# Optimization experiments

Measured on AMD Instinct MI355X. Metric: run time of the kernel, lower is better.

## Reference

```python
import jax, jax.numpy as jnp
import numpy as np

N_NODES = 50000


def spmm(rows, cols, vals, dense):
    # out[i,:] = sum_{e: rows[e]==i} vals[e] * dense[cols[e], :]
    gathered = dense[cols] * vals[:, None]  # [E, D]
    return jax.ops.segment_sum(gathered, rows, num_segments=N_NODES)


def setup_inputs() -> dict:
    key = jax.random.key(0)
    k1, k2, k3, k4, k5, k6 = jax.random.split(key, 6)
    N, E, F, H, C = N_NODES, 800000, 512, 256, 64
    node_features = jax.random.normal(k1, (N, F), dtype=jnp.float32)
    adj_rows = jax.random.randint(k2, (E,), 0, N, dtype=jnp.int32)
    adj_cols = jax.random.randint(k3, (E,), 0, N, dtype=jnp.int32)
    adj_vals = jax.random.uniform(k4, (E,), dtype=jnp.float32)
    W1 = jax.random.normal(k5, (F, H), dtype=jnp.float32) * (1.0 / np.sqrt(F))
    b1 = jnp.zeros((H,), dtype=jnp.float32)
    W2 = jax.random.normal(k6, (H, C), dtype=jnp.float32) * (1.0 / np.sqrt(H))
    b2 = jnp.zeros((C,), dtype=jnp.float32)
    return {"node_features": node_features, "adj_rows": adj_rows,
            "adj_cols": adj_cols, "adj_vals": adj_vals,
            "W1": W1, "b1": b1, "W2": W2, "b2": b2}


def reference(node_features, adj_rows, adj_cols, adj_vals, W1, b1, W2, b2):
    # Layer 1: dense projection then sparse aggregation, then ReLU.
    support1 = node_features @ W1 + b1           # [N, H]
    x = jax.nn.relu(spmm(adj_rows, adj_cols, adj_vals, support1))
    # Dropout is identity in eval mode (training=False).
    # Layer 2
    support2 = x @ W2 + b2                       # [N, C]
    x = spmm(adj_rows, adj_cols, adj_vals, support2)
    return jax.nn.log_softmax(x, axis=1)
```

## Files before the change

kernel.cpp:

```cpp
#include <hip/hip_runtime.h>

#define N_NODES 50000
#define N_EDGES 800000
#define F_IN    512
#define H_DIM   256
#define C_DIM   64
#define MPAD    50048

#define NB      196
#define NCHUNK  196
#define CHUNK   4096
#define BCAP    6144

typedef __bf16 bf16;
typedef __bf16 bf16x4 __attribute__((ext_vector_type(4)));
typedef __bf16 bf16x8 __attribute__((ext_vector_type(8)));
typedef float  f32x4  __attribute__((ext_vector_type(4)));
typedef unsigned int u32;
typedef unsigned long long u64;
typedef unsigned char u8;

__device__ __forceinline__ void gl_lds16(const void* g, void* l) {
    __builtin_amdgcn_global_load_lds(
        (const __attribute__((address_space(1))) u32*)g,
        (__attribute__((address_space(3))) u32*)l, 16, 0, 0);
}

__device__ __forceinline__ float unpack_val(u32 pk) {
    return __builtin_bit_cast(float, pk << 16);
}


__global__ __launch_bounds__(1024) void prep_k(const int* __restrict__ rows,
                                               const float* __restrict__ W1,
                                               const float* __restrict__ W2,
                                               u32* __restrict__ G,
                                               bf16* __restrict__ W1t,
                                               bf16* __restrict__ W2t) {
    __shared__ u32 h[16 * NB];
    int bid = blockIdx.x, tid = threadIdx.x;
    if (bid < NCHUNK) {
        int wid = tid >> 6;
        for (int i = tid; i < 16 * NB; i += 1024) h[i] = 0;
        __syncthreads();
        int base = bid * CHUNK;
        int end = base + CHUNK; if (end > N_EDGES) end = N_EDGES;
        for (int e = base + tid; e < end; e += 1024)
            atomicAdd(&h[wid * NB + (rows[e] >> 8)], 1);
        __syncthreads();
        if (tid < NB) {
            u32 s = 0;
#pragma unroll
            for (int w = 0; w < 16; w++) s += h[w * NB + tid];
            G[tid * NCHUNK + bid] = s;
        }
    } else {
        int i = (bid - NCHUNK) * 1024 + tid;
        if (i < F_IN * H_DIM) {
            int k = i >> 8, n = i & 255;
            W1t[n * F_IN + k] = (bf16)W1[i];
        } else {
            int j = i - F_IN * H_DIM;
            if (j < H_DIM * C_DIM) {
                int k = j >> 6, n = j & 63;
                W2t[n * H_DIM + k] = (bf16)W2[j];
            }
        }
    }
}


__global__ __launch_bounds__(512) void sg_k(const int* __restrict__ rows,
                                            const int* __restrict__ cols,
                                            const float* __restrict__ vals,
                                            const u32* __restrict__ G,
                                            u32* __restrict__ epack,
                                            u8* __restrict__ lrow,
                                            const float* __restrict__ A,
                                            const bf16* __restrict__ Bt,
                                            const float* __restrict__ bias,
                                            bf16* __restrict__ C) {
    __shared__ __attribute__((aligned(16))) char smem[49152];
    int bid = blockIdx.x, tid = threadIdx.x;
    int wid = tid >> 6, lane = tid & 63;

    if (bid < NCHUNK) {
        u32* sdat  = (u32*)smem;
        u8*  sbkt  = (u8*)(smem + 16384);
        u8*  srow  = (u8*)(smem + 20480);
        u32* h     = (u32*)(smem + 24576);
        u32* loff  = (u32*)(smem + 32768);
        u32* lcur  = (u32*)(smem + 33792);
        u32* gbase = (u32*)(smem + 34816);
        u32* wt    = (u32*)(smem + 35840);
        int c = bid;
        int base = c * CHUNK;
        int end = base + CHUNK; if (end > N_EDGES) end = N_EDGES;
        int n = end - base;

        for (int i = tid; i < 2048; i += 512) h[i] = 0;

        u32 tot = 0, pre = 0, incl = 0;
        if (tid < 256) {
            if (tid < NB) {
                for (int cc = 0; cc < NCHUNK; cc++) {
                    u32 v = G[tid * NCHUNK + cc];
                    tot += v;
                    if (cc < c) pre += v;
                }
            }
            incl = tot;
#pragma unroll
            for (int off = 1; off < 64; off <<= 1) {
                u32 u = __shfl_up(incl, off, 64);
                if (lane >= off) incl += u;
            }
            if (lane == 63) wt[wid] = incl;
        }
        __syncthreads();
        if (tid < 256) {
            u32 wpre = 0;
#pragma unroll
            for (int w = 0; w < 4; w++)
                if (w < wid) wpre += wt[w];
            if (tid < NB) gbase[tid] = (wpre + incl - tot) + pre;
        }

        u32 pk_r[8], b_r[8], lr_r[8];
#pragma unroll
        for (int j = 0; j < 8; j++) {
            int e = base + tid + j * 512;
            bool ok = e < end;
            int ee = ok ? e : base;
            int r = rows[ee];
            unsigned short vb = __builtin_bit_cast(unsigned short, (bf16)vals[ee]);
            pk_r[j] = ((u32)cols[ee] << 16) | (u32)vb;
            b_r[j] = (u32)(r >> 8);
            lr_r[j] = (u32)(r & 255);
            if (ok) atomicAdd(&h[wid * 256 + b_r[j]], 1);
        }
        __syncthreads();

        u32 t2 = 0, incl2 = 0;
        if (tid < 256) {
#pragma unroll
            for (int w2 = 0; w2 < 8; w2++) t2 += h[w2 * 256 + tid];
            incl2 = t2;
#pragma unroll
            for (int off = 1; off < 64; off <<= 1) {
                u32 u = __shfl_up(incl2, off, 64);
                if (lane >= off) incl2 += u;
            }
            if (lane == 63) wt[wid] = incl2;
        }
        __syncthreads();
        if (tid < 256) {
            u32 wpre2 = 0;
#pragma unroll
            for (int w = 0; w < 4; w++)
                if (w < wid) wpre2 += wt[w];
            u32 excl = wpre2 + incl2 - t2;
            loff[tid] = excl;
            lcur[tid] = excl;
        }
        __syncthreads();

#pragma unroll
        for (int j = 0; j < 8; j++) {
            int e = base + tid + j * 512;
            if (e < end) {
                u32 p = atomicAdd(&lcur[b_r[j]], 1);
                sdat[p] = pk_r[j];
                sbkt[p] = (u8)b_r[j];
                srow[p] = (u8)lr_r[j];
            }
        }
        __syncthreads();

        for (int i = tid; i < n; i += 512) {
            u32 b2 = sbkt[i];
            u32 dst = gbase[b2] + (u32)i - loff[b2];
            epack[dst] = sdat[i];
            lrow[dst] = srow[i];
        }
        return;
    }

    constexpr int BM = 128, BK = 64;
    bf16* As = (bf16*)smem;
    bf16* Bs = (bf16*)(smem + 16384);
    int wr = wid >> 2, wc = wid & 3;
    int l15 = lane & 15, hi = lane >> 4;
    int sw = l15 & 7;
    int bm = bid - NCHUNK;

    f32x4 acc[4][4];
#pragma unroll
    for (int m = 0; m < 4; m++)
#pragma unroll
        for (int n = 0; n < 4; n++) acc[m][n] = (f32x4){0.f, 0.f, 0.f, 0.f};

    for (int kt = 0; kt < F_IN; kt += BK) {
#pragma unroll
        for (int j = 0; j < 4; j++) {
            int ch = j * 512 + tid;
            int row = ch >> 3, kc = ch & 7;
            int kcs = kc ^ (row & 7);
            gl_lds16(Bt + (size_t)row * F_IN + kt + kcs * 8,
                     &Bs[(j * 512 + wid * 64) * 8]);
        }
#pragma unroll
        for (int j = 0; j < 2; j++) {
            int ch = j * 512 + tid;
            int row = ch >> 3, kc = ch & 7;
            int ar = bm * BM + row;
            if (ar >= N_NODES) ar = N_NODES - 1;
            const f32x4* src = (const f32x4*)(A + (size_t)ar * F_IN + kt + kc * 8);
            f32x4 u = src[0], v = src[1];
            bf16x8 o;
            o[0] = (bf16)u[0]; o[1] = (bf16)u[1]; o[2] = (bf16)u[2]; o[3] = (bf16)u[3];
            o[4] = (bf16)v[0]; o[5] = (bf16)v[1]; o[6] = (bf16)v[2]; o[7] = (bf16)v[3];
            *(bf16x8*)&As[row * BK + (kc ^ (row & 7)) * 8] = o;
        }
        __syncthreads();

        bf16x8 afr[2][4], bfr[2][4];
#pragma unroll
        for (int kk = 0; kk < 2; kk++) {
            int c = (kk * 4 + hi) ^ sw;
#pragma unroll
            for (int m = 0; m < 4; m++)
                afr[kk][m] = *(const bf16x8*)&As[(wr * 64 + m * 16 + l15) * BK + c * 8];
#pragma unroll
            for (int n = 0; n < 4; n++)
                bfr[kk][n] = *(const bf16x8*)&Bs[(wc * 64 + n * 16 + l15) * BK + c * 8];
        }
#pragma unroll
        for (int kk = 0; kk < 2; kk++)
#pragma unroll
            for (int m = 0; m < 4; m++)
#pragma unroll
                for (int n = 0; n < 4; n++)
                    acc[m][n] = __builtin_amdgcn_mfma_f32_16x16x32_bf16(
                        afr[kk][m], bfr[kk][n], acc[m][n], 0, 0, 0);
        __syncthreads();
    }

#pragma unroll
    for (int m = 0; m < 4; m++) {
        int row0 = bm * BM + wr * 64 + m * 16 + hi * 4;
#pragma unroll
        for (int n = 0; n < 4; n++) {
            int col = wc * 64 + n * 16 + l15;
            float bz = bias[col];
#pragma unroll
            for (int r = 0; r < 4; r++) {
                int row = row0 + r;
                if (row < N_NODES)
                    C[(size_t)row * H_DIM + col] = (bf16)(acc[m][n][r] + bz);
            }
        }
    }
}


__global__ __launch_bounds__(256) void sortC_k(u32* __restrict__ epack,
                                               const u8* __restrict__ lrow,
                                               const u32* __restrict__ G,
                                               int* __restrict__ starts) {
    __shared__ u32 edat[BCAP];
    __shared__ u32 sdat[BCAP];
    __shared__ u8  erow[BCAP];
    __shared__ u32 h[4 * 256];
    __shared__ u32 cur[256];
    __shared__ u32 wt1[4], wt2[4];
    __shared__ u32 sh_s, sh_n;
    int b = blockIdx.x, tid = threadIdx.x, wid = tid >> 6, lane = tid & 63;

    u32 btot = 0;
    if (tid < NB)
        for (int cc = 0; cc < NCHUNK; cc++) btot += G[tid * NCHUNK + cc];
    u32 bincl = btot;
#pragma unroll
    for (int off = 1; off < 64; off <<= 1) {
        u32 u = __shfl_up(bincl, off, 64);
        if (lane >= off) bincl += u;
    }
    if (lane == 63) wt1[wid] = bincl;
    __syncthreads();
    u32 bwpre = 0;
#pragma unroll
    for (int w = 0; w < 4; w++)
        if (w < wid) bwpre += wt1[w];
    if (tid == b) { sh_s = bwpre + bincl - btot; sh_n = btot; }
    __syncthreads();
    int s = (int)sh_s;
    int n = (int)sh_n;
    if (n > BCAP) n = BCAP;

    for (int i = tid; i < n; i += 256) { edat[i] = epack[s + i]; erow[i] = lrow[s + i]; }
    for (int i = tid; i < 1024; i += 256) h[i] = 0;
    __syncthreads();
    for (int i = tid; i < n; i += 256) atomicAdd(&h[wid * 256 + erow[i]], 1);
    __syncthreads();
    u32 tot = h[tid] + h[256 + tid] + h[512 + tid] + h[768 + tid];
    u32 incl = tot;
#pragma unroll
    for (int off = 1; off < 64; off <<= 1) {
        u32 u = __shfl_up(incl, off, 64);
        if (lane >= off) incl += u;
    }
    if (lane == 63) wt2[wid] = incl;
    __syncthreads();
    u32 wpre = 0;
#pragma unroll
    for (int w = 0; w < 4; w++)
        if (w < wid) wpre += wt2[w];
    u32 excl = wpre + incl - tot;
    cur[tid] = excl;
    int grow = b * 256 + tid;
    if (grow < N_NODES) starts[grow] = s + (int)excl;
    if (b == 0 && tid == 0) starts[N_NODES] = N_EDGES;
    __syncthreads();
    for (int i = tid; i < n; i += 256) {
        u32 p = atomicAdd(&cur[erow[i]], 1);
        sdat[p] = edat[i];
    }
    __syncthreads();
    for (int i = tid; i < n; i += 256) epack[s + i] = sdat[i];
}


__global__ __launch_bounds__(256) void gemm2_k(const bf16* __restrict__ A,
                                               const bf16* __restrict__ Bt,
                                               const float* __restrict__ bias,
                                               bf16* __restrict__ C) {
    constexpr int BM = 128, BK = 64;
    __shared__ bf16 As[BM * BK];
    __shared__ bf16 Bs[64 * BK];

    int tid = threadIdx.x;
    int wid = tid >> 6, lane = tid & 63;
    int wr = wid >> 1, wc = wid & 1;
    int l15 = lane & 15, hi = lane >> 4;
    int sw = l15 & 7;
    int bm = blockIdx.x;

    f32x4 acc[4][2];
#pragma unroll
    for (int m = 0; m < 4; m++)
#pragma unroll
        for (int n = 0; n < 2; n++) acc[m][n] = (f32x4){0.f, 0.f, 0.f, 0.f};

    for (int kt = 0; kt < H_DIM; kt += BK) {
#pragma unroll
        for (int j = 0; j < 4; j++) {
            int ch = j * 256 + tid;
            int row = ch >> 3, kc = ch & 7;
            int kcs = kc ^ (row & 7);
            gl_lds16(A + (size_t)(bm * BM + row) * H_DIM + kt + kcs * 8,
                     &As[(j * 256 + wid * 64) * 8]);
        }
#pragma unroll
        for (int j = 0; j < 2; j++) {
            int ch = j * 256 + tid;
            int row = ch >> 3, kc = ch & 7;
            int kcs = kc ^ (row & 7);
            gl_lds16(Bt + (size_t)row * H_DIM + kt + kcs * 8,
                     &Bs[(j * 256 + wid * 64) * 8]);
        }
        __syncthreads();

        bf16x8 afr[2][4], bfr[2][2];
#pragma unroll
        for (int kk = 0; kk < 2; kk++) {
            int c = (kk * 4 + hi) ^ sw;
#pragma unroll
            for (int m = 0; m < 4; m++)
                afr[kk][m] = *(const bf16x8*)&As[(wr * 64 + m * 16 + l15) * BK + c * 8];
#pragma unroll
            for (int n = 0; n < 2; n++)
                bfr[kk][n] = *(const bf16x8*)&Bs[(wc * 32 + n * 16 + l15) * BK + c * 8];
        }
#pragma unroll
        for (int kk = 0; kk < 2; kk++)
#pragma unroll
            for (int m = 0; m < 4; m++)
#pragma unroll
                for (int n = 0; n < 2; n++)
                    acc[m][n] = __builtin_amdgcn_mfma_f32_16x16x32_bf16(
                        afr[kk][m], bfr[kk][n], acc[m][n], 0, 0, 0);
        __syncthreads();
    }

#pragma unroll
    for (int m = 0; m < 4; m++) {
        int row0 = bm * BM + wr * 64 + m * 16 + hi * 4;
#pragma unroll
        for (int n = 0; n < 2; n++) {
            int col = wc * 32 + n * 16 + l15;
            float bz = bias[col];
#pragma unroll
            for (int r = 0; r < 4; r++) {
                int row = row0 + r;
                if (row < N_NODES)
                    C[(size_t)row * C_DIM + col] = (bf16)(acc[m][n][r] + bz);
            }
        }
    }
}


__global__ __launch_bounds__(256) void spmm1_k(const int* __restrict__ starts,
                                               const u32* __restrict__ epack,
                                               const bf16* __restrict__ s1,
                                               bf16* __restrict__ x16) {
    int wid = threadIdx.x >> 6, lane = threadIdx.x & 63;
    int row = blockIdx.x * 4 + wid;
    if (row >= N_NODES) return;
    int s = starts[row], e = starts[row + 1];
    f32x4 acc = (f32x4){0.f, 0.f, 0.f, 0.f};
    const bf16* s1l = s1 + lane * 4;
    int p = s;
    for (; p + 8 <= e; p += 8) {
        u32 k0 = __builtin_nontemporal_load(epack + p);
        u32 k1 = __builtin_nontemporal_load(epack + p + 1);
        u32 k2 = __builtin_nontemporal_load(epack + p + 2);
        u32 k3 = __builtin_nontemporal_load(epack + p + 3);
        u32 k4 = __builtin_nontemporal_load(epack + p + 4);
        u32 k5 = __builtin_nontemporal_load(epack + p + 5);
        u32 k6 = __builtin_nontemporal_load(epack + p + 6);
        u32 k7 = __builtin_nontemporal_load(epack + p + 7);
        bf16x4 g0 = *(const bf16x4*)(s1l + (size_t)(k0 >> 16) * H_DIM);
        bf16x4 g1 = *(const bf16x4*)(s1l + (size_t)(k1 >> 16) * H_DIM);
        bf16x4 g2 = *(const bf16x4*)(s1l + (size_t)(k2 >> 16) * H_DIM);
        bf16x4 g3 = *(const bf16x4*)(s1l + (size_t)(k3 >> 16) * H_DIM);
        bf16x4 g4 = *(const bf16x4*)(s1l + (size_t)(k4 >> 16) * H_DIM);
        bf16x4 g5 = *(const bf16x4*)(s1l + (size_t)(k5 >> 16) * H_DIM);
        bf16x4 g6 = *(const bf16x4*)(s1l + (size_t)(k6 >> 16) * H_DIM);
        bf16x4 g7 = *(const bf16x4*)(s1l + (size_t)(k7 >> 16) * H_DIM);
        float v0 = unpack_val(k0), v1 = unpack_val(k1), v2 = unpack_val(k2), v3 = unpack_val(k3);
        float v4 = unpack_val(k4), v5 = unpack_val(k5), v6 = unpack_val(k6), v7 = unpack_val(k7);
#pragma unroll
        for (int j = 0; j < 4; j++)
            acc[j] += v0 * (float)g0[j] + v1 * (float)g1[j] +
                      v2 * (float)g2[j] + v3 * (float)g3[j] +
                      v4 * (float)g4[j] + v5 * (float)g5[j] +
                      v6 * (float)g6[j] + v7 * (float)g7[j];
    }
    for (; p < e; ++p) {
        u32 k = __builtin_nontemporal_load(epack + p);
        float v = unpack_val(k);
        bf16x4 g = *(const bf16x4*)(s1l + (size_t)(k >> 16) * H_DIM);
#pragma unroll
        for (int j = 0; j < 4; j++) acc[j] += v * (float)g[j];
    }
    bf16x4 o;
#pragma unroll
    for (int j = 0; j < 4; j++) o[j] = (bf16)fmaxf(acc[j], 0.f);
    u64 bits = __builtin_bit_cast(u64, o);
    __builtin_nontemporal_store(bits, (u64*)(x16 + (size_t)row * H_DIM + lane * 4));
}


__global__ __launch_bounds__(256) void spmm2_sm_k(const int* __restrict__ starts,
                                                  const u32* __restrict__ epack,
                                                  const bf16* __restrict__ s2,
                                                  float* __restrict__ out) {
    int wid = threadIdx.x >> 6, lane = threadIdx.x & 63;
    int row = blockIdx.x * 4 + wid;
    if (row >= N_NODES) return;
    int s = starts[row], e = starts[row + 1];
    float acc = 0.f;
    int p = s;
    for (; p + 8 <= e; p += 8) {
        u32 k0 = __builtin_nontemporal_load(epack + p);
        u32 k1 = __builtin_nontemporal_load(epack + p + 1);
        u32 k2 = __builtin_nontemporal_load(epack + p + 2);
        u32 k3 = __builtin_nontemporal_load(epack + p + 3);
        u32 k4 = __builtin_nontemporal_load(epack + p + 4);
        u32 k5 = __builtin_nontemporal_load(epack + p + 5);
        u32 k6 = __builtin_nontemporal_load(epack + p + 6);
        u32 k7 = __builtin_nontemporal_load(epack + p + 7);
        float g0 = (float)s2[(size_t)(k0 >> 16) * C_DIM + lane];
        float g1 = (float)s2[(size_t)(k1 >> 16) * C_DIM + lane];
        float g2 = (float)s2[(size_t)(k2 >> 16) * C_DIM + lane];
        float g3 = (float)s2[(size_t)(k3 >> 16) * C_DIM + lane];
        float g4 = (float)s2[(size_t)(k4 >> 16) * C_DIM + lane];
        float g5 = (float)s2[(size_t)(k5 >> 16) * C_DIM + lane];
        float g6 = (float)s2[(size_t)(k6 >> 16) * C_DIM + lane];
        float g7 = (float)s2[(size_t)(k7 >> 16) * C_DIM + lane];
        acc += unpack_val(k0) * g0 + unpack_val(k1) * g1 +
               unpack_val(k2) * g2 + unpack_val(k3) * g3 +
               unpack_val(k4) * g4 + unpack_val(k5) * g5 +
               unpack_val(k6) * g6 + unpack_val(k7) * g7;
    }
    for (; p < e; ++p) {
        u32 k = __builtin_nontemporal_load(epack + p);
        acc += unpack_val(k) * (float)s2[(size_t)(k >> 16) * C_DIM + lane];
    }
    float mx = acc;
#pragma unroll
    for (int off = 32; off >= 1; off >>= 1) mx = fmaxf(mx, __shfl_xor(mx, off, 64));
    float ex = expf(acc - mx);
    float se = ex;
#pragma unroll
    for (int off = 32; off >= 1; off >>= 1) se += __shfl_xor(se, off, 64);
    __builtin_nontemporal_store((acc - mx) - logf(se),
                                out + (size_t)row * C_DIM + lane);
}


extern "C" void kernel_launch(void* const* d_in, const int* in_sizes, int n_in,
                              void* d_out, int out_size, void* d_ws, size_t ws_size,
                              hipStream_t stream) {
    const float* nf   = (const float*)d_in[0];
    const int*   rows = (const int*)d_in[1];
    const int*   cols = (const int*)d_in[2];
    const float* vals = (const float*)d_in[3];
    const float* W1   = (const float*)d_in[4];
    const float* b1   = (const float*)d_in[5];
    const float* W2   = (const float*)d_in[6];
    const float* b2   = (const float*)d_in[7];
    float* out = (float*)d_out;

    char* w = (char*)d_ws;
    auto alloc = [&](size_t b) { void* p = (void*)w; w += (b + 255) & ~(size_t)255; return p; };

    bf16* x16  = (bf16*)alloc((size_t)MPAD * H_DIM * 2);
    bf16* sup1 = (bf16*)alloc((size_t)N_NODES * H_DIM * 2);
    bf16* sup2 = sup1;
    bf16* W1t = (bf16*)alloc((size_t)H_DIM * F_IN * 2);
    bf16* W2t = (bf16*)alloc((size_t)C_DIM * H_DIM * 2);
    int* starts = (int*)alloc((size_t)(N_NODES + 1) * 4);
    u32* G      = (u32*)alloc((size_t)NB * NCHUNK * 4);
    u32* epack  = (u32*)alloc((size_t)N_EDGES * 4);
    u8*  lrow   = (u8*)alloc((size_t)N_EDGES);

    prep_k<<<NCHUNK + 144, 1024, 0, stream>>>(rows, W1, W2, G, W1t, W2t);
    sg_k<<<NCHUNK + MPAD / 128, 512, 0, stream>>>(rows, cols, vals, G, epack, lrow,
                                                  nf, W1t, b1, sup1);
    sortC_k<<<NB, 256, 0, stream>>>(epack, lrow, G, starts);
    spmm1_k<<<(N_NODES + 3) / 4, 256, 0, stream>>>(starts, epack, sup1, x16);
    gemm2_k<<<MPAD / 128, 256, 0, stream>>>(x16, W2t, b2, sup2);
    spmm2_sm_k<<<(N_NODES + 3) / 4, 256, 0, stream>>>(starts, epack, sup2, out);

    (void)in_sizes; (void)n_in; (void)out_size; (void)ws_size;
}
```

Before: 172.3 us.

## Halve GEMM1 row tile to 64 and double-buffer edge staging arrays

The fused scatter/GEMM kernel's GEMM path moves from 128-row to 64-row tiles. Each of the 8 waves now covers all 64 rows and 32 output columns, and the launch grows to twice as many GEMM blocks with less shared memory per block. This should improve occupancy and load balance across CUs, at the cost of reloading the W1 tile more often. The edge bucketing output also moves to separate staging buffers, so the sort kernel reads from one array and writes to another instead of working in place, which costs extra workspace.

```diff
diff --git a/kernel.cpp b/kernel.cpp
--- a/kernel.cpp
+++ b/kernel.cpp
@@ -74,13 +74,13 @@
                                             const int* __restrict__ cols,
                                             const float* __restrict__ vals,
                                             const u32* __restrict__ G,
-                                            u32* __restrict__ epack,
-                                            u8* __restrict__ lrow,
+                                            u32* __restrict__ epckS,
+                                            u8* __restrict__ lrowS,
                                             const float* __restrict__ A,
                                             const bf16* __restrict__ Bt,
                                             const float* __restrict__ bias,
                                             bf16* __restrict__ C) {
-    __shared__ __attribute__((aligned(16))) char smem[49152];
+    __shared__ __attribute__((aligned(16))) char smem[40960];
     int bid = blockIdx.x, tid = threadIdx.x;
     int wid = tid >> 6, lane = tid & 63;
 
@@ -180,25 +180,24 @@
         for (int i = tid; i < n; i += 512) {
             u32 b2 = sbkt[i];
             u32 dst = gbase[b2] + (u32)i - loff[b2];
-            epack[dst] = sdat[i];
-            lrow[dst] = srow[i];
+            epckS[dst] = sdat[i];
+            lrowS[dst] = srow[i];
         }
         return;
     }
 
-    constexpr int BM = 128, BK = 64;
+    constexpr int BM = 64, BK = 64;
     bf16* As = (bf16*)smem;
-    bf16* Bs = (bf16*)(smem + 16384);
-    int wr = wid >> 2, wc = wid & 3;
+    bf16* Bs = (bf16*)(smem + 8192);
     int l15 = lane & 15, hi = lane >> 4;
     int sw = l15 & 7;
     int bm = bid - NCHUNK;
 
-    f32x4 acc[4][4];
+    f32x4 acc[4][2];
 #pragma unroll
     for (int m = 0; m < 4; m++)
 #pragma unroll
-        for (int n = 0; n < 4; n++) acc[m][n] = (f32x4){0.f, 0.f, 0.f, 0.f};
+        for (int n = 0; n < 2; n++) acc[m][n] = (f32x4){0.f, 0.f, 0.f, 0.f};
 
     for (int kt = 0; kt < F_IN; kt += BK) {
 #pragma unroll
@@ -209,10 +208,8 @@
             gl_lds16(Bt + (size_t)row * F_IN + kt + kcs * 8,
                      &Bs[(j * 512 + wid * 64) * 8]);
         }
-#pragma unroll
-        for (int j = 0; j < 2; j++) {
-            int ch = j * 512 + tid;
-            int row = ch >> 3, kc = ch & 7;
+        {
+            int row = tid >> 3, kc = tid & 7;
             int ar = bm * BM + row;
             if (ar >= N_NODES) ar = N_NODES - 1;
             const f32x4* src = (const f32x4*)(A + (size_t)ar * F_IN + kt + kc * 8);
@@ -224,23 +221,23 @@
         }
         __syncthreads();
 
-        bf16x8 afr[2][4], bfr[2][4];
+        bf16x8 afr[2][4], bfr[2][2];
 #pragma unroll
         for (int kk = 0; kk < 2; kk++) {
             int c = (kk * 4 + hi) ^ sw;
 #pragma unroll
             for (int m = 0; m < 4; m++)
-                afr[kk][m] = *(const bf16x8*)&As[(wr * 64 + m * 16 + l15) * BK + c * 8];
-#pragma unroll
-            for (int n = 0; n < 4; n++)
-                bfr[kk][n] = *(const bf16x8*)&Bs[(wc * 64 + n * 16 + l15) * BK + c * 8];
+                afr[kk][m] = *(const bf16x8*)&As[(m * 16 + l15) * BK + c * 8];
+#pragma unroll
+            for (int n = 0; n < 2; n++)
+                bfr[kk][n] = *(const bf16x8*)&Bs[(wid * 32 + n * 16 + l15) * BK + c * 8];
         }
 #pragma unroll
         for (int kk = 0; kk < 2; kk++)
 #pragma unroll
             for (int m = 0; m < 4; m++)
 #pragma unroll
-                for (int n = 0; n < 4; n++)
+                for (int n = 0; n < 2; n++)
                     acc[m][n] = __builtin_amdgcn_mfma_f32_16x16x32_bf16(
                         afr[kk][m], bfr[kk][n], acc[m][n], 0, 0, 0);
         __syncthreads();
@@ -248,10 +245,10 @@
 
 #pragma unroll
     for (int m = 0; m < 4; m++) {
-        int row0 = bm * BM + wr * 64 + m * 16 + hi * 4;
-#pragma unroll
-        for (int n = 0; n < 4; n++) {
-            int col = wc * 64 + n * 16 + l15;
+        int row0 = bm * BM + m * 16 + hi * 4;
+#pragma unroll
+        for (int n = 0; n < 2; n++) {
+            int col = wid * 32 + n * 16 + l15;
             float bz = bias[col];
 #pragma unroll
             for (int r = 0; r < 4; r++) {
@@ -264,9 +261,10 @@
 }
 
 
-__global__ __launch_bounds__(256) void sortC_k(u32* __restrict__ epack,
-                                               const u8* __restrict__ lrow,
+__global__ __launch_bounds__(256) void sortC_k(const u32* __restrict__ epckS,
+                                               const u8* __restrict__ lrowS,
                                                const u32* __restrict__ G,
+                                               u32* __restrict__ epack,
                                                int* __restrict__ starts) {
     __shared__ u32 edat[BCAP];
     __shared__ u32 sdat[BCAP];
@@ -298,7 +296,7 @@
     int n = (int)sh_n;
     if (n > BCAP) n = BCAP;
 
-    for (int i = tid; i < n; i += 256) { edat[i] = epack[s + i]; erow[i] = lrow[s + i]; }
+    for (int i = tid; i < n; i += 256) { edat[i] = epckS[s + i]; erow[i] = lrowS[s + i]; }
     for (int i = tid; i < 1024; i += 256) h[i] = 0;
     __syncthreads();
     for (int i = tid; i < n; i += 256) atomicAdd(&h[wid * 256 + erow[i]], 1);
@@ -535,12 +533,13 @@
     int* starts = (int*)alloc((size_t)(N_NODES + 1) * 4);
     u32* G      = (u32*)alloc((size_t)NB * NCHUNK * 4);
     u32* epack  = (u32*)alloc((size_t)N_EDGES * 4);
-    u8*  lrow   = (u8*)alloc((size_t)N_EDGES);
+    u32* epckS  = (u32*)alloc((size_t)N_EDGES * 4);
+    u8*  lrowS  = (u8*)alloc((size_t)N_EDGES);
 
     prep_k<<<NCHUNK + 144, 1024, 0, stream>>>(rows, W1, W2, G, W1t, W2t);
-    sg_k<<<NCHUNK + MPAD / 128, 512, 0, stream>>>(rows, cols, vals, G, epack, lrow,
-                                                  nf, W1t, b1, sup1);
-    sortC_k<<<NB, 256, 0, stream>>>(epack, lrow, G, starts);
+    sg_k<<<NCHUNK + MPAD / 64, 512, 0, stream>>>(rows, cols, vals, G, epckS, lrowS,
+                                                 nf, W1t, b1, sup1);
+    sortC_k<<<NB, 256, 0, stream>>>(epckS, lrowS, G, epack, starts);
     spmm1_k<<<(N_NODES + 3) / 4, 256, 0, stream>>>(starts, epack, sup1, x16);
     gemm2_k<<<MPAD / 128, 256, 0, stream>>>(x16, W2t, b2, sup2);
     spmm2_sm_k<<<(N_NODES + 3) / 4, 256, 0, stream>>>(starts, epack, sup2, out);
```

Result: faster. 166.2 us (-3.5%).
